# Kernel optimization log

Hardware: AMD Instinct MI355X
Metric: run time of the kernel (lower is better)

Reference implementation:

```python
import jax, jax.numpy as jnp
import numpy as np

HIDDEN = 1024
STATE = 16
DT_RANK = 64


def setup_inputs() -> dict:
    key = jax.random.key(0)
    ks = jax.random.split(key, 5)
    B, S = 2, 2048
    x = jax.random.normal(ks[0], (B, S, HIDDEN), dtype=jnp.float32)
    # lecun_normal-ish init scales
    W_xproj = jax.random.normal(ks[1], (HIDDEN, STATE * 2 + DT_RANK), dtype=jnp.float32) / np.sqrt(HIDDEN)
    W_dt = jax.random.normal(ks[2], (DT_RANK, HIDDEN), dtype=jnp.float32) / np.sqrt(DT_RANK)
    b_dt = jnp.zeros((HIDDEN,), dtype=jnp.float32)
    A_log = jax.random.normal(ks[3], (STATE, HIDDEN), dtype=jnp.float32) / np.sqrt(STATE)
    return {"x": x, "W_xproj": W_xproj, "W_dt": W_dt, "b_dt": b_dt, "A_log": A_log}


def reference(x, W_xproj, W_dt, b_dt, A_log):
    # x: [B, S, D]
    xp = x @ W_xproj                       # [B, S, 2N + R]
    Bm = xp[..., :STATE]                    # [B, S, N]
    Cm = xp[..., STATE:2 * STATE]           # [B, S, N]
    dt = jax.nn.softplus(xp[..., 2 * STATE:] @ W_dt + b_dt)  # [B, S, D]
    A = -jnp.exp(A_log)                     # [N, D]
    A_bar = jnp.exp(A[None, None] * dt[:, :, None, :])        # [B, S, N, D]
    Bu = Bm[:, :, :, None] * dt[:, :, None, :] * x[:, :, None, :]  # [B, S, N, D]

    def scan_fn(h, inp):
        A_t, Bu_t = inp
        h = A_t * h + Bu_t
        return h, h

    h0 = jnp.zeros(Bu.shape[:1] + Bu.shape[2:], dtype=x.dtype)   # [B, N, D]
    _, h_all = jax.lax.scan(scan_fn, h0,
                            (A_bar.transpose(1, 0, 2, 3), Bu.transpose(1, 0, 2, 3)))  # [S, B, N, D]
    y = jnp.einsum('bsn,sbnd->bsd', Cm, h_all)  # [B, S, D]
    return y
```

## Files before the change

kernel.cpp:

```cpp
#include <hip/hip_runtime.h>
#include <math.h>

#define HIDDEN 1024
#define NSTATE 16
#define DTRANK 64
#define BB 2
#define SS 2048
#define ROWS (BB*SS)
#define XPC 96
#define CH 128
#define CL 16
#define BND (BB*NSTATE*HIDDEN)
#define LOG2E 1.44269504088896f

#define RT 64
#define KSPL 8
#define RX (ROWS*XPC)

__global__ __launch_bounds__(256) void k_xproj2(const float* __restrict__ x,
                                                const float* __restrict__ W,
                                                float* __restrict__ part) {
    __shared__ float xs[RT * 32];
    __shared__ float wt[96 * 36];
    int t  = threadIdx.x;
    int rt = blockIdx.x >> 3;
    int ks = blockIdx.x & 7;
    int r0 = rt * RT;
    int k0 = ks * 128;
    int cg = t & 15, rg = t >> 4;

    float acc[4][6];
    #pragma unroll
    for (int a = 0; a < 4; ++a)
        #pragma unroll
        for (int b = 0; b < 6; ++b) acc[a][b] = 0.f;

    for (int ch = 0; ch < 4; ++ch) {
        int kc = k0 + ch * 32;
        __syncthreads();
        #pragma unroll
        for (int m = 0; m < 2; ++m) {
            int e = t + m * 256;
            int row = e >> 3, kb = e & 7;
            float4 v = *(const float4*)&x[(r0 + row) * HIDDEN + kc + kb * 4];
            int kbp = kb ^ ((row >> 2) & 7);
            *(float4*)&xs[row * 32 + kbp * 4] = v;
        }
        #pragma unroll
        for (int m = 0; m < 3; ++m) {
            int f = t + m * 256;
            int kr = f / 24, cq = f % 24;
            float4 v = *(const float4*)&W[(kc + kr) * XPC + cq * 4];
            wt[(cq * 4 + 0) * 36 + kr] = v.x;
            wt[(cq * 4 + 1) * 36 + kr] = v.y;
            wt[(cq * 4 + 2) * 36 + kr] = v.z;
            wt[(cq * 4 + 3) * 36 + kr] = v.w;
        }
        __syncthreads();
        #pragma unroll
        for (int kg = 0; kg < 8; ++kg) {
            float4 wv[6], xv[4];
            #pragma unroll
            for (int j = 0; j < 6; ++j)
                wv[j] = *(float4*)&wt[(cg + 16 * j) * 36 + kg * 4];
            #pragma unroll
            for (int rr = 0; rr < 4; ++rr) {
                int row = rg * 4 + rr;
                xv[rr] = *(float4*)&xs[row * 32 + ((kg ^ ((row >> 2) & 7)) * 4)];
            }
            #pragma unroll
            for (int rr = 0; rr < 4; ++rr)
                #pragma unroll
                for (int j = 0; j < 6; ++j) {
                    acc[rr][j] = fmaf(xv[rr].x, wv[j].x, acc[rr][j]);
                    acc[rr][j] = fmaf(xv[rr].y, wv[j].y, acc[rr][j]);
                    acc[rr][j] = fmaf(xv[rr].z, wv[j].z, acc[rr][j]);
                    acc[rr][j] = fmaf(xv[rr].w, wv[j].w, acc[rr][j]);
                }
        }
    }
    #pragma unroll
    for (int rr = 0; rr < 4; ++rr)
        #pragma unroll
        for (int j = 0; j < 6; ++j)
            part[ks * RX + (r0 + rg * 4 + rr) * XPC + cg + 16 * j] = acc[rr][j];
}

__global__ void k_reduce(const float* __restrict__ part, float* __restrict__ xp) {
    int i = (blockIdx.x * 256 + threadIdx.x) * 4;
    float4 s = *(const float4*)&part[i];
    #pragma unroll
    for (int p = 1; p < KSPL; ++p) {
        float4 v = *(const float4*)&part[p * RX + i];
        s.x += v.x; s.y += v.y; s.z += v.z; s.w += v.w;
    }
    *(float4*)&xp[i] = s;
}

__global__ __launch_bounds__(256) void k_dt3(const float* __restrict__ xp,
                                             const float* __restrict__ Wdt,
                                             const float* __restrict__ bdt,
                                             float* __restrict__ dt) {
    __shared__ float xs[8 * 64];
    int t = threadIdx.x;
    int r0 = (blockIdx.x >> 2) * 8;
    int col = (blockIdx.x & 3) * 256 + t;
    if (t < 128) {
        int row = t >> 4, kq = t & 15;
        *(float4*)&xs[row * 64 + kq * 4] =
            *(const float4*)&xp[(r0 + row) * XPC + 2 * NSTATE + kq * 4];
    }
    __syncthreads();
    float acc[8];
    float b = bdt[col];
    #pragma unroll
    for (int rr = 0; rr < 8; ++rr) acc[rr] = b;
    #pragma unroll 8
    for (int k = 0; k < DTRANK; ++k) {
        float w = Wdt[k * HIDDEN + col];
        #pragma unroll
        for (int rr = 0; rr < 8; ++rr)
            acc[rr] = fmaf(xs[rr * 64 + k], w, acc[rr]);
    }
    #pragma unroll
    for (int rr = 0; rr < 8; ++rr) {
        float a = acc[rr];
        float o = fmaxf(a, 0.f) + __logf(1.f + __expf(-fabsf(a)));
        dt[(r0 + rr) * HIDDEN + col] = o;
    }
}

__global__ __launch_bounds__(256, 4)
void k_pass1(const float* __restrict__ x, const float* __restrict__ dt,
             const float* __restrict__ xp, const float* __restrict__ Alog,
             float* __restrict__ P, float* __restrict__ Q) {
    int bid = blockIdx.x;
    int dblk = bid & 3;
    int b = (bid >> 2) & 1;
    int c = bid >> 3;
    int d = dblk * 256 + threadIdx.x;
    float A2[NSTATE], Pv[NSTATE], Qv[NSTATE];
    #pragma unroll
    for (int n = 0; n < NSTATE; ++n) {
        A2[n] = -__expf(Alog[n*HIDDEN + d]) * LOG2E;
        Pv[n] = 1.f; Qv[n] = 0.f;
    }
    int s0 = c * CL;
    #pragma unroll 4
    for (int i = 0; i < CL; ++i) {
        int r = b*SS + s0 + i;
        float dv = dt[r*HIDDEN + d];
        float xv = x[r*HIDDEN + d];
        float bm[NSTATE];
        *(float4*)&bm[0]  = *(const float4*)&xp[r*XPC + 0];
        *(float4*)&bm[4]  = *(const float4*)&xp[r*XPC + 4];
        *(float4*)&bm[8]  = *(const float4*)&xp[r*XPC + 8];
        *(float4*)&bm[12] = *(const float4*)&xp[r*XPC + 12];
        float bx = dv * xv;
        #pragma unroll
        for (int n = 0; n < NSTATE; ++n) {
            float a = exp2f(A2[n] * dv);
            Qv[n] = fmaf(a, Qv[n], bm[n] * bx);
            Pv[n] *= a;
        }
    }
    int base = b*(NSTATE*HIDDEN) + d;
    #pragma unroll
    for (int n = 0; n < NSTATE; ++n) {
        P[c*BND + base + n*HIDDEN] = Pv[n];
        Q[c*BND + base + n*HIDDEN] = Qv[n];
    }
}

__global__ void k_pass2(float* __restrict__ P, const float* __restrict__ Q) {
    int bnd = blockIdx.x * 256 + threadIdx.x;
    float h = 0.f;
    for (int cb = 0; cb < CH / 16; ++cb) {
        float p[16], q[16];
        #pragma unroll
        for (int j = 0; j < 16; ++j) {
            int idx = (cb*16 + j)*BND + bnd;
            p[j] = P[idx]; q[j] = Q[idx];
        }
        #pragma unroll
        for (int j = 0; j < 16; ++j) {
            int idx = (cb*16 + j)*BND + bnd;
            P[idx] = h;
            h = fmaf(p[j], h, q[j]);
        }
    }
}

__global__ __launch_bounds__(256, 4)
void k_pass3(const float* __restrict__ x, const float* __restrict__ dt,
             const float* __restrict__ xp, const float* __restrict__ Alog,
             const float* __restrict__ Hs, float* __restrict__ y) {
    int bid = blockIdx.x;
    int dblk = bid & 3;
    int b = (bid >> 2) & 1;
    int c = bid >> 3;
    int d = dblk * 256 + threadIdx.x;

    float A2[NSTATE], h[NSTATE];
    #pragma unroll
    for (int n = 0; n < NSTATE; ++n) {
        A2[n] = -__expf(Alog[n*HIDDEN + d]) * LOG2E;
        h[n] = Hs[c*BND + b*(NSTATE*HIDDEN) + n*HIDDEN + d];
    }
    int s0 = c * CL;
    #pragma unroll 2
    for (int i = 0; i < CL; ++i) {
        int r = b*SS + s0 + i;
        float dv = dt[r*HIDDEN + d];
        float xv = x[r*HIDDEN + d];
        float bx = dv * xv;
        float bm[NSTATE], cm[NSTATE];
        *(float4*)&bm[0]  = *(const float4*)&xp[r*XPC + 0];
        *(float4*)&bm[4]  = *(const float4*)&xp[r*XPC + 4];
        *(float4*)&bm[8]  = *(const float4*)&xp[r*XPC + 8];
        *(float4*)&bm[12] = *(const float4*)&xp[r*XPC + 12];
        *(float4*)&cm[0]  = *(const float4*)&xp[r*XPC + 16];
        *(float4*)&cm[4]  = *(const float4*)&xp[r*XPC + 20];
        *(float4*)&cm[8]  = *(const float4*)&xp[r*XPC + 24];
        *(float4*)&cm[12] = *(const float4*)&xp[r*XPC + 28];
        float yv = 0.f;
        #pragma unroll
        for (int n = 0; n < NSTATE; ++n) {
            float a = exp2f(A2[n] * dv);
            h[n] = fmaf(a, h[n], bm[n] * bx);
            yv = fmaf(cm[n], h[n], yv);
        }
        y[r*HIDDEN + d] = yv;
    }
}

extern "C" void kernel_launch(void* const* d_in, const int* in_sizes, int n_in,
                              void* d_out, int out_size, void* d_ws, size_t ws_size,
                              hipStream_t stream) {
    const float* x    = (const float*)d_in[0];
    const float* Wx   = (const float*)d_in[1];
    const float* Wdt  = (const float*)d_in[2];
    const float* bdt  = (const float*)d_in[3];
    const float* Alog = (const float*)d_in[4];
    float* y  = (float*)d_out;
    float* ws = (float*)d_ws;

    float* xp   = ws;
    float* dt   = xp + RX;
    float* part = dt + ROWS*HIDDEN;
    float* P    = part + (size_t)KSPL*RX;
    float* Q    = P + (size_t)CH*BND;

    k_xproj2<<<(ROWS/RT)*KSPL, 256, 0, stream>>>(x, Wx, part);
    k_reduce<<<RX/4/256, 256, 0, stream>>>(part, xp);
    k_dt3<<<(ROWS/8)*4, 256, 0, stream>>>(xp, Wdt, bdt, dt);
    k_pass1<<<CH*BB*4, 256, 0, stream>>>(x, dt, xp, Alog, P, Q);
    k_pass2<<<BND/256, 256, 0, stream>>>(P, Q);
    k_pass3<<<CH*BB*4, 256, 0, stream>>>(x, dt, xp, Alog, P, y);
}
```

Baseline: 116.9 us.

## Fuse split-K reduce, dt projection and chunk pass1 into one kernel

Merges the partial-sum reduction, the dt low-rank projection with softplus, and the first chunked-scan pass into a single kernel. Each block reduces the xproj partials for its chunk into shared memory and computes dt in registers, so pass1 no longer rereads dt and the B columns from global memory. Chunk count is halved and chunk length doubled so the fused kernel has more rows per block. The trade-offs are half as many blocks, heavier per-thread register use (32 dt values plus state), the reduction repeated by all four d-blocks, and a serial pass2 that now runs over fewer chunks.

```diff
diff --git a/kernel.cpp b/kernel.cpp
--- a/kernel.cpp
+++ b/kernel.cpp
@@ -8,8 +8,8 @@
 #define SS 2048
 #define ROWS (BB*SS)
 #define XPC 96
-#define CH 128
-#define CL 16
+#define CH 64
+#define CL 32
 #define BND (BB*NSTATE*HIDDEN)
 #define LOG2E 1.44269504088896f
 
@@ -86,85 +86,74 @@
             part[ks * RX + (r0 + rg * 4 + rr) * XPC + cg + 16 * j] = acc[rr][j];
 }
 
-__global__ void k_reduce(const float* __restrict__ part, float* __restrict__ xp) {
-    int i = (blockIdx.x * 256 + threadIdx.x) * 4;
-    float4 s = *(const float4*)&part[i];
-    #pragma unroll
-    for (int p = 1; p < KSPL; ++p) {
-        float4 v = *(const float4*)&part[p * RX + i];
-        s.x += v.x; s.y += v.y; s.z += v.z; s.w += v.w;
-    }
-    *(float4*)&xp[i] = s;
-}
-
-__global__ __launch_bounds__(256) void k_dt3(const float* __restrict__ xp,
-                                             const float* __restrict__ Wdt,
-                                             const float* __restrict__ bdt,
-                                             float* __restrict__ dt) {
-    __shared__ float xs[8 * 64];
+__global__ __launch_bounds__(256)
+void k_fused2(const float* __restrict__ part, const float* __restrict__ Wdt,
+              const float* __restrict__ bdt, const float* __restrict__ x,
+              const float* __restrict__ Alog, float* __restrict__ xp,
+              float* __restrict__ dt, float* __restrict__ P,
+              float* __restrict__ Q) {
+    __shared__ float lx[CL * XPC];
     int t = threadIdx.x;
-    int r0 = (blockIdx.x >> 2) * 8;
-    int col = (blockIdx.x & 3) * 256 + t;
-    if (t < 128) {
-        int row = t >> 4, kq = t & 15;
-        *(float4*)&xs[row * 64 + kq * 4] =
-            *(const float4*)&xp[(r0 + row) * XPC + 2 * NSTATE + kq * 4];
-    }
-    __syncthreads();
-    float acc[8];
-    float b = bdt[col];
-    #pragma unroll
-    for (int rr = 0; rr < 8; ++rr) acc[rr] = b;
-    #pragma unroll 8
-    for (int k = 0; k < DTRANK; ++k) {
-        float w = Wdt[k * HIDDEN + col];
-        #pragma unroll
-        for (int rr = 0; rr < 8; ++rr)
-            acc[rr] = fmaf(xs[rr * 64 + k], w, acc[rr]);
-    }
-    #pragma unroll
-    for (int rr = 0; rr < 8; ++rr) {
-        float a = acc[rr];
-        float o = fmaxf(a, 0.f) + __logf(1.f + __expf(-fabsf(a)));
-        dt[(r0 + rr) * HIDDEN + col] = o;
-    }
-}
-
-__global__ __launch_bounds__(256, 4)
-void k_pass1(const float* __restrict__ x, const float* __restrict__ dt,
-             const float* __restrict__ xp, const float* __restrict__ Alog,
-             float* __restrict__ P, float* __restrict__ Q) {
     int bid = blockIdx.x;
     int dblk = bid & 3;
     int b = (bid >> 2) & 1;
     int c = bid >> 3;
-    int d = dblk * 256 + threadIdx.x;
+    int row0 = b * SS + c * CL;
+    int d = dblk * 256 + t;
+
+    #pragma unroll
+    for (int m = 0; m < CL * XPC / 256; ++m) {
+        int e = t + m * 256;
+        int rl = e / XPC, col = e % XPC;
+        int gi = (row0 + rl) * XPC + col;
+        float s = 0.f;
+        #pragma unroll
+        for (int p = 0; p < KSPL; ++p) s += part[p * RX + gi];
+        lx[e] = s;
+        if (dblk == 0) xp[gi] = s;
+    }
+    __syncthreads();
+
+    float dtv[CL];
+    {
+        float bv = bdt[d];
+        #pragma unroll
+        for (int rr = 0; rr < CL; ++rr) dtv[rr] = bv;
+        #pragma unroll 4
+        for (int k = 0; k < DTRANK; ++k) {
+            float w = Wdt[k * HIDDEN + d];
+            #pragma unroll
+            for (int rr = 0; rr < CL; ++rr)
+                dtv[rr] = fmaf(lx[rr * XPC + 2 * NSTATE + k], w, dtv[rr]);
+        }
+        #pragma unroll
+        for (int rr = 0; rr < CL; ++rr) {
+            float a = dtv[rr];
+            float o = fmaxf(a, 0.f) + __logf(1.f + __expf(-fabsf(a)));
+            dtv[rr] = o;
+            dt[(row0 + rr) * HIDDEN + d] = o;
+        }
+    }
+
     float A2[NSTATE], Pv[NSTATE], Qv[NSTATE];
     #pragma unroll
     for (int n = 0; n < NSTATE; ++n) {
         A2[n] = -__expf(Alog[n*HIDDEN + d]) * LOG2E;
         Pv[n] = 1.f; Qv[n] = 0.f;
     }
-    int s0 = c * CL;
-    #pragma unroll 4
+    #pragma unroll 2
     for (int i = 0; i < CL; ++i) {
-        int r = b*SS + s0 + i;
-        float dv = dt[r*HIDDEN + d];
-        float xv = x[r*HIDDEN + d];
-        float bm[NSTATE];
-        *(float4*)&bm[0]  = *(const float4*)&xp[r*XPC + 0];
-        *(float4*)&bm[4]  = *(const float4*)&xp[r*XPC + 4];
-        *(float4*)&bm[8]  = *(const float4*)&xp[r*XPC + 8];
-        *(float4*)&bm[12] = *(const float4*)&xp[r*XPC + 12];
+        float dv = dtv[i];
+        float xv = x[(row0 + i) * HIDDEN + d];
         float bx = dv * xv;
         #pragma unroll
         for (int n = 0; n < NSTATE; ++n) {
             float a = exp2f(A2[n] * dv);
-            Qv[n] = fmaf(a, Qv[n], bm[n] * bx);
+            Qv[n] = fmaf(a, Qv[n], lx[i * XPC + n] * bx);
             Pv[n] *= a;
         }
     }
-    int base = b*(NSTATE*HIDDEN) + d;
+    int base = b * (NSTATE * HIDDEN) + d;
     #pragma unroll
     for (int n = 0; n < NSTATE; ++n) {
         P[c*BND + base + n*HIDDEN] = Pv[n];
@@ -252,9 +241,7 @@
     float* Q    = P + (size_t)CH*BND;
 
     k_xproj2<<<(ROWS/RT)*KSPL, 256, 0, stream>>>(x, Wx, part);
-    k_reduce<<<RX/4/256, 256, 0, stream>>>(part, xp);
-    k_dt3<<<(ROWS/8)*4, 256, 0, stream>>>(xp, Wdt, bdt, dt);
-    k_pass1<<<CH*BB*4, 256, 0, stream>>>(x, dt, xp, Alog, P, Q);
+    k_fused2<<<CH*BB*4, 256, 0, stream>>>(part, Wdt, bdt, x, Alog, xp, dt, P, Q);
     k_pass2<<<BND/256, 256, 0, stream>>>(P, Q);
     k_pass3<<<CH*BB*4, 256, 0, stream>>>(x, dt, xp, Alog, P, y);
 }
```

Measured after the change: 105.6 us. -9.7%, faster.
